# Optimization experiments

Measured on AMD Instinct MI355X. Metric: run time of the kernel, lower is better.

Reference implementation:

```python
import jax, jax.numpy as jnp
import numpy as np

# Dims: B=32 batch, C=64 feat channels, Np=192 priors, No=72 row offsets,
# Ns=36 pooled sample points (maxpool kernel 2), Hd=64 fc hidden.
B, C, Np, No, Hd = 32, 64, 192, 72, 64
NS_POOL = 2  # n_offsets // sample_points
REG_DIM = No + 4  # reg_layers output


def bilinear_sample(feat, gx, gy):
    """torch F.grid_sample(align_corners=True) equivalent for in-range coords.
    feat: [B,C,H,W]; gx,gy: [B,Np,S] normalized to [-1,1]. -> [B,C,Np,S]."""
    Bb, Cc, H, W = feat.shape
    ix = (gx + 1.0) * 0.5 * (W - 1)
    iy = (gy + 1.0) * 0.5 * (H - 1)
    ix0f = jnp.floor(ix); iy0f = jnp.floor(iy)
    wx = ix - ix0f; wy = iy - iy0f
    ix0 = jnp.clip(ix0f.astype(jnp.int32), 0, W - 1)
    iy0 = jnp.clip(iy0f.astype(jnp.int32), 0, H - 1)
    ix1 = jnp.clip(ix0 + 1, 0, W - 1)
    iy1 = jnp.clip(iy0 + 1, 0, H - 1)
    ff = feat.reshape(Bb, Cc, H * W)
    S = gx.shape[1] * gx.shape[2]
    def gather(iy_, ix_):
        idx = (iy_ * W + ix_).reshape(Bb, 1, S)
        g = jnp.take_along_axis(ff, jnp.broadcast_to(idx, (Bb, Cc, S)), axis=2)
        return g.reshape(Bb, Cc, gx.shape[1], gx.shape[2])
    v00 = gather(iy0, ix0); v01 = gather(iy0, ix1)
    v10 = gather(iy1, ix0); v11 = gather(iy1, ix1)
    wx = wx[:, None]; wy = wy[:, None]  # broadcast over C
    return (v00 * (1 - wx) * (1 - wy) + v01 * wx * (1 - wy)
            + v10 * (1 - wx) * wy + v11 * wx * wy)


def _mlp2(h, Ws, bs):
    # two stacked Linear+ReLU layers (num_fc=2)
    for i in range(2):
        h = jax.nn.relu(h @ Ws[i] + bs[i])
    return h


def setup_inputs() -> dict:
    key = jax.random.key(0)
    ks = jax.random.split(key, 24)
    w = lambda k, sh: jax.random.normal(k, sh, dtype=jnp.float32) * 0.05
    return {
        "x0": jax.random.normal(ks[0], (B, C, 40, 100), dtype=jnp.float32),
        "x1": jax.random.normal(ks[1], (B, C, 20, 50), dtype=jnp.float32),
        "x2": jax.random.normal(ks[2], (B, C, 10, 25), dtype=jnp.float32),
        "prior_xs0": jax.random.uniform(ks[3], (Np, No), dtype=jnp.float32),
        "l_weight": w(ks[4], (No,)),              # self.l embedding, sigmoid gate
        "lsgi_w": w(ks[5], (3, C, C)),            # per-stage lsgi projection
        "fc_w": w(ks[6], (C, Hd)), "fc_b": w(ks[7], (Hd,)),
        "cls_w": w(ks[8], (2, Hd, Hd)), "cls_b": w(ks[9], (2, Hd)),
        "cls_ow": w(ks[10], (Hd, 2)), "cls_ob": w(ks[11], (2,)),
        "reg_w": w(ks[12], (2, Hd, Hd)), "reg_b": w(ks[13], (2, Hd)),
        "reg_ow": w(ks[14], (Hd, REG_DIM)), "reg_ob": w(ks[15], (REG_DIM,)),
        "loc_w": w(ks[16], (2, Hd, Hd)), "loc_b": w(ks[17], (2, Hd)),
        "loc_ow": w(ks[18], (Hd, 1)), "loc_ob": w(ks[19], (1,)),
    }


def reference(x0, x1, x2, prior_xs0, l_weight, lsgi_w, fc_w, fc_b,
              cls_w, cls_b, cls_ow, cls_ob, reg_w, reg_b, reg_ow, reg_ob,
              loc_w, loc_b, loc_ow, loc_ob):
    pyramid = [x2, x1, x0]  # reversed: coarsest level first (stage 0)
    prior_feat_ys = jnp.linspace(1.0, 0.0, No, dtype=jnp.float32)
    gy = jnp.broadcast_to((prior_feat_ys * 2.0 - 1.0)[None, None, :], (B, Np, No))
    prior_xs = jnp.broadcast_to(prior_xs0[None], (B, Np, No))
    gate = jax.nn.sigmoid(l_weight)[:, None]  # [No,1]
    stage_feats = []
    outs = []
    for s in range(3):
        gx = prior_xs * 2.0 - 1.0
        pooled = bilinear_sample(pyramid[s], gx, gy)          # [B,C,Np,No]
        pooled = jnp.transpose(pooled, (0, 2, 3, 1)) * gate   # [B,Np,No,C]
        pooled = jax.nn.relu(jnp.einsum('bnoc,cd->bnod', pooled, lsgi_w[s]))
        # MaxPool2d kernel (2,1) over the offset axis -> Ns=36 sample points
        comp = pooled.reshape(B, Np, No // NS_POOL, NS_POOL, C).max(axis=3)
        stage_feats.append(comp)
        # cross-stage fusion (global head): mean over stages and sample points
        fused = jnp.stack(stage_feats, 0).mean(axis=0).mean(axis=2)  # [B,Np,C]
        fc = jax.nn.relu(fused @ fc_w + fc_b)                        # [B,Np,Hd]
        cls = _mlp2(fc, cls_w, cls_b) @ cls_ow + cls_ob              # [B,Np,2]
        reg = _mlp2(fc, reg_w, reg_b) @ reg_ow + reg_ob              # [B,Np,No+4]
        loc = _mlp2(fc, loc_w, loc_b) @ loc_ow + loc_ob              # [B,Np,1]
        outs.append(jnp.concatenate([cls, reg, loc], axis=-1))      # [B,Np,79]
        # refine anchors for next stage from predicted xs
        prior_xs = jax.nn.sigmoid(reg[..., 4:])
    return jnp.stack(outs, axis=0)  # [3,B,Np,79]
```

## Files before the change

kernel.cpp:

```cpp
#include <hip/hip_runtime.h>
#include <hip/hip_bf16.h>

#define Bq   32
#define Cq   64
#define NPq  192
#define NOq  72
#define PTS  (NPq * NOq)
#define REGD 76
#define OUTD 79

typedef __attribute__((ext_vector_type(8))) short short8;
typedef __attribute__((ext_vector_type(4))) float float4v;

__device__ inline unsigned short f2bf(float x) {
    __hip_bfloat16 h = __float2bfloat16(x);
    return *reinterpret_cast<unsigned short*>(&h);
}

__global__ __launch_bounds__(256) void build_tables_kernel(
    const float* __restrict__ f0,
    const float* __restrict__ f1,
    const float* __restrict__ f2,
    const float* __restrict__ lw,
    unsigned short* __restrict__ t0,
    unsigned short* __restrict__ t1,
    unsigned short* __restrict__ t2)
{
    __shared__ float sRow[64 * 101];

    const int tid = threadIdx.x;
    const int o   = blockIdx.x / 96;
    const int sb  = blockIdx.x - o * 96;
    const int s   = sb >> 5;
    const int b   = sb & 31;

    const float* feat; unsigned short* tab; int H, W;
    if (s == 0)      { feat = f0; tab = t0; H = 10; W = 25; }
    else if (s == 1) { feat = f1; tab = t1; H = 20; W = 50; }
    else             { feat = f2; tab = t2; H = 40; W = 100; }
    const int Wp = W + 1;

    const float ys = 1.0f - (float)o * (1.0f / 71.0f);
    const float iy = ys * (float)(H - 1);
    const float fy = floorf(iy);
    const float wy = iy - fy;
    int iy0 = (int)fy; iy0 = iy0 < 0 ? 0 : (iy0 > H - 1 ? H - 1 : iy0);
    const int iy1 = (iy0 + 1 > H - 1) ? H - 1 : iy0 + 1;
    const float gate = 1.0f / (1.0f + __expf(-lw[o]));

    const float* fb = feat + (size_t)b * 64 * H * W;
    const int iy0W = iy0 * W, iy1W = iy1 * W;

    const int tot = 64 * W;
    for (int idx = tid; idx < tot; idx += 256) {
        const int c = idx / W;
        const int x = idx - c * W;
        const float* f = fb + c * (H * W);
        sRow[c * Wp + x] = ((1.0f - wy) * f[iy0W + x] + wy * f[iy1W + x]) * gate;
    }
    __syncthreads();

    unsigned short* to = tab + (size_t)(b * NOq + o) * Wp * 64;
    const int tot2 = Wp * 64;
    for (int idx = tid; idx < tot2; idx += 256) {
        const int x = idx >> 6;
        const int c = idx & 63;
        const int xx = (x < W) ? x : (W - 1);
        to[idx] = f2bf(sRow[c * Wp + xx]);
    }
}

template<int W>
__global__ __launch_bounds__(256) void fused_pool_head_kernel(
    const unsigned short* __restrict__ tab,
    const float* __restrict__ xsrc, const int xstride,
    const float* __restrict__ lsgi,
    float* __restrict__ sumFeat,
    const int stage,
    const float* __restrict__ fc_w,  const float* __restrict__ fc_b,
    const float* __restrict__ cls_w, const float* __restrict__ cls_b,
    const float* __restrict__ cls_ow, const float* __restrict__ cls_ob,
    const float* __restrict__ reg_w, const float* __restrict__ reg_b,
    const float* __restrict__ reg_ow, const float* __restrict__ reg_ob,
    const float* __restrict__ loc_w, const float* __restrict__ loc_b,
    const float* __restrict__ loc_ow, const float* __restrict__ loc_ob,
    float* __restrict__ out, float* __restrict__ xs_next)
{
    constexpr int Wp = W + 1;
    __shared__ __align__(16) float sF  [8][68];
    __shared__ __align__(16) float bufC[8][64];
    __shared__ __align__(16) float bufA[8][64];
    __shared__ __align__(16) float bufB[8][64];

    const int tid  = threadIdx.x;
    const int w    = tid >> 6;
    const int lane = tid & 63;
    const int ng   = blockIdx.x >> 5;
    const int b    = blockIdx.x & 31;
    const int npair = ng * 4 + w;

    short8 wf[4][2];
    {
        const int kb = ((lane >> 4) & 3) * 8;
        const int dl = lane & 15;
        #pragma unroll
        for (int ks = 0; ks < 2; ++ks)
            #pragma unroll
            for (int dt = 0; dt < 4; ++dt) {
                union { unsigned short u[8]; short8 v; } pk;
                #pragma unroll
                for (int j = 0; j < 8; ++j)
                    pk.u[j] = f2bf(lsgi[(ks * 32 + kb + j) * 64 + dt * 16 + dl]);
                wf[dt][ks] = pk.v;
            }
    }

    const unsigned short* tb = tab + (size_t)b * NOq * Wp * 64;
    const float* xp = xsrc + (size_t)xstride * b;
    const int m  = lane & 15;
    const int kg = lane >> 4;
    const int nt0 = npair * 9;

    float sums0[4] = {0.f, 0.f, 0.f, 0.f};
    float sums1[4] = {0.f, 0.f, 0.f, 0.f};

    #pragma unroll
    for (int ntl = 0; ntl < 9; ++ntl) {
        const int pt = (nt0 + ntl) * 16 + m;
        const int o  = pt % NOq;
        float ixf = xp[pt] * (float)(W - 1);
        ixf = fminf(fmaxf(ixf, 0.0f), (float)(W - 1));
        const float fx = floorf(ixf);
        const float wx = ixf - fx;
        const int ix0 = (int)fx;

        const unsigned short* col = tb + ((size_t)o * Wp + ix0) * 64 + kg * 8;
        const short8 a00 = *(const short8*)(col);
        const short8 a01 = *(const short8*)(col + 64);
        const short8 a10 = *(const short8*)(col + 32);
        const short8 a11 = *(const short8*)(col + 96);

        float wxr[4];
        #pragma unroll
        for (int j = 0; j < 4; ++j) wxr[j] = __shfl(wx, kg * 4 + j);

        const bool hi = (ntl * 16 + (kg * 4)) >= NOq;
        #pragma unroll
        for (int dt = 0; dt < 4; ++dt) {
            float4v c0 = {0.f, 0.f, 0.f, 0.f};
            float4v c1 = {0.f, 0.f, 0.f, 0.f};
            c0 = __builtin_amdgcn_mfma_f32_16x16x32_bf16(a00, wf[dt][0], c0, 0, 0, 0);
            c0 = __builtin_amdgcn_mfma_f32_16x16x32_bf16(a10, wf[dt][1], c0, 0, 0, 0);
            c1 = __builtin_amdgcn_mfma_f32_16x16x32_bf16(a01, wf[dt][0], c1, 0, 0, 0);
            c1 = __builtin_amdgcn_mfma_f32_16x16x32_bf16(a11, wf[dt][1], c1, 0, 0, 0);
            const float v0 = c0[0] + wxr[0] * (c1[0] - c0[0]);
            const float v1 = c0[1] + wxr[1] * (c1[1] - c0[1]);
            const float v2 = c0[2] + wxr[2] * (c1[2] - c0[2]);
            const float v3 = c0[3] + wxr[3] * (c1[3] - c0[3]);
            const float pm0 = fmaxf(fmaxf(v0, v1), 0.f);
            const float pm1 = fmaxf(fmaxf(v2, v3), 0.f);
            const float add = pm0 + pm1;
            if (hi) sums1[dt] += add; else sums0[dt] += add;
        }
    }

    #pragma unroll
    for (int dt = 0; dt < 4; ++dt) {
        float v0 = sums0[dt], v1 = sums1[dt];
        v0 += __shfl_xor(v0, 16); v0 += __shfl_xor(v0, 32);
        v1 += __shfl_xor(v1, 16); v1 += __shfl_xor(v1, 32);
        sums0[dt] = v0; sums1[dt] = v1;
    }

    const float invS = 1.0f / (float)(stage + 1);
    if (lane < 16) {
        const size_t row0 = (size_t)(b * NPq + npair * 2) * 64;
        #pragma unroll
        for (int dt = 0; dt < 4; ++dt) {
            const int d = dt * 16 + lane;
            float t0 = sums0[dt] * (1.0f / 36.0f);
            float t1 = sums1[dt] * (1.0f / 36.0f);
            float* p0 = sumFeat + row0 + d;
            float* p1 = sumFeat + row0 + 64 + d;
            if (stage > 0) { t0 += *p0; t1 += *p1; }
            *p0 = t0; *p1 = t1;
            sF[2 * w][d]     = t0 * invS;
            sF[2 * w + 1][d] = t1 * invS;
        }
    }
    __syncthreads();

    const int pA  = w;
    const int pB  = w + 4;
    const int p0g = b * NPq + ng * 8;

    auto layer = [&](const float* iA, const float* iB, float* oA, float* oB,
                     const float* __restrict__ gw, const float* __restrict__ gb) {
        const float bias = gb[lane];
        float accA = bias, accB = bias;
        #pragma unroll 4
        for (int k = 0; k < 64; k += 4) {
            const float4 a4 = *(const float4*)(iA + k);
            const float4 b4 = *(const float4*)(iB + k);
            const float w0 = gw[(k + 0) * 64 + lane];
            const float w1 = gw[(k + 1) * 64 + lane];
            const float w2 = gw[(k + 2) * 64 + lane];
            const float w3 = gw[(k + 3) * 64 + lane];
            accA += a4.x * w0 + a4.y * w1 + a4.z * w2 + a4.w * w3;
            accB += b4.x * w0 + b4.y * w1 + b4.z * w2 + b4.w * w3;
        }
        oA[lane] = fmaxf(accA, 0.f);
        oB[lane] = fmaxf(accB, 0.f);
        __builtin_amdgcn_wave_barrier();
    };

    layer(sF[pA], sF[pB], bufC[pA], bufC[pB], fc_w, fc_b);

    layer(bufC[pA], bufC[pB], bufA[pA], bufA[pB], cls_w,        cls_b);
    layer(bufA[pA], bufA[pB], bufB[pA], bufB[pB], cls_w + 4096, cls_b + 64);
    {
        const float bA = bufB[pA][lane], bB = bufB[pB][lane];
        const float2 ow = *(const float2*)&cls_ow[lane * 2];
        float v0 = bA * ow.x, v1 = bA * ow.y;
        float v2 = bB * ow.x, v3 = bB * ow.y;
        #pragma unroll
        for (int m2 = 1; m2 < 64; m2 <<= 1) {
            v0 += __shfl_xor(v0, m2);
            v1 += __shfl_xor(v1, m2);
            v2 += __shfl_xor(v2, m2);
            v3 += __shfl_xor(v3, m2);
        }
        if (lane == 0) {
            out[(size_t)(p0g + pA) * OUTD + 0] = v0 + cls_ob[0];
            out[(size_t)(p0g + pA) * OUTD + 1] = v1 + cls_ob[1];
            out[(size_t)(p0g + pB) * OUTD + 0] = v2 + cls_ob[0];
            out[(size_t)(p0g + pB) * OUTD + 1] = v3 + cls_ob[1];
        }
    }

    layer(bufC[pA], bufC[pB], bufA[pA], bufA[pB], reg_w,        reg_b);
    layer(bufA[pA], bufA[pB], bufB[pA], bufB[pB], reg_w + 4096, reg_b + 64);
    {
        const int j1 = lane;
        const int j2 = (lane < 12) ? 64 + lane : 75;
        float zA1 = reg_ob[j1], zB1 = zA1;
        float zA2 = reg_ob[j2], zB2 = zA2;
        #pragma unroll 4
        for (int k = 0; k < 64; k += 4) {
            const float4 a4 = *(const float4*)&bufB[pA][k];
            const float4 b4 = *(const float4*)&bufB[pB][k];
            const float u0 = reg_ow[(k + 0) * REGD + j1];
            const float u1 = reg_ow[(k + 1) * REGD + j1];
            const float u2 = reg_ow[(k + 2) * REGD + j1];
            const float u3 = reg_ow[(k + 3) * REGD + j1];
            const float t0 = reg_ow[(k + 0) * REGD + j2];
            const float t1 = reg_ow[(k + 1) * REGD + j2];
            const float t2 = reg_ow[(k + 2) * REGD + j2];
            const float t3 = reg_ow[(k + 3) * REGD + j2];
            zA1 += a4.x * u0 + a4.y * u1 + a4.z * u2 + a4.w * u3;
            zB1 += b4.x * u0 + b4.y * u1 + b4.z * u2 + b4.w * u3;
            zA2 += a4.x * t0 + a4.y * t1 + a4.z * t2 + a4.w * t3;
            zB2 += b4.x * t0 + b4.y * t1 + b4.z * t2 + b4.w * t3;
        }
        float* orA = out + (size_t)(p0g + pA) * OUTD;
        float* orB = out + (size_t)(p0g + pB) * OUTD;
        float* xsA = xs_next + (size_t)(p0g + pA) * NOq;
        float* xsB = xs_next + (size_t)(p0g + pB) * NOq;
        orA[2 + j1] = zA1;
        orB[2 + j1] = zB1;
        if (lane >= 4) {
            xsA[j1 - 4] = 1.0f / (1.0f + __expf(-zA1));
            xsB[j1 - 4] = 1.0f / (1.0f + __expf(-zB1));
        }
        if (lane < 12) {
            orA[2 + j2] = zA2;
            orB[2 + j2] = zB2;
            xsA[j2 - 4] = 1.0f / (1.0f + __expf(-zA2));
            xsB[j2 - 4] = 1.0f / (1.0f + __expf(-zB2));
        }
    }

    layer(bufC[pA], bufC[pB], bufA[pA], bufA[pB], loc_w,        loc_b);
    layer(bufA[pA], bufA[pB], bufB[pA], bufB[pB], loc_w + 4096, loc_b + 64);
    {
        float v0 = bufB[pA][lane] * loc_ow[lane];
        float v1 = bufB[pB][lane] * loc_ow[lane];
        #pragma unroll
        for (int m2 = 1; m2 < 64; m2 <<= 1) {
            v0 += __shfl_xor(v0, m2);
            v1 += __shfl_xor(v1, m2);
        }
        if (lane == 0) {
            out[(size_t)(p0g + pA) * OUTD + 78] = v0 + loc_ob[0];
            out[(size_t)(p0g + pB) * OUTD + 78] = v1 + loc_ob[0];
        }
    }
}

extern "C" void kernel_launch(void* const* d_in, const int* in_sizes, int n_in,
                              void* d_out, int out_size, void* d_ws, size_t ws_size,
                              hipStream_t stream)
{
    const float* x0        = (const float*)d_in[0];
    const float* x1        = (const float*)d_in[1];
    const float* x2        = (const float*)d_in[2];
    const float* prior_xs0 = (const float*)d_in[3];
    const float* l_weight  = (const float*)d_in[4];
    const float* lsgi_w    = (const float*)d_in[5];
    const float* fc_w      = (const float*)d_in[6];
    const float* fc_b      = (const float*)d_in[7];
    const float* cls_w     = (const float*)d_in[8];
    const float* cls_b     = (const float*)d_in[9];
    const float* cls_ow    = (const float*)d_in[10];
    const float* cls_ob    = (const float*)d_in[11];
    const float* reg_w     = (const float*)d_in[12];
    const float* reg_b     = (const float*)d_in[13];
    const float* reg_ow    = (const float*)d_in[14];
    const float* reg_ob    = (const float*)d_in[15];
    const float* loc_w     = (const float*)d_in[16];
    const float* loc_b     = (const float*)d_in[17];
    const float* loc_ow    = (const float*)d_in[18];
    const float* loc_ob    = (const float*)d_in[19];

    float* out     = (float*)d_out;
    float* sumFeat = (float*)d_ws;
    float* xs      = sumFeat + (size_t)Bq * NPq * Cq;
    unsigned short* tab0 = (unsigned short*)(xs + (size_t)Bq * PTS);
    unsigned short* tab1 = tab0 + (size_t)Bq * NOq * 26  * 64;
    unsigned short* tab2 = tab1 + (size_t)Bq * NOq * 51  * 64;

    hipLaunchKernelGGL(build_tables_kernel, dim3(3 * Bq * NOq), dim3(256), 0, stream,
                       x2, x1, x0, l_weight, tab0, tab1, tab2);

    for (int s = 0; s < 3; ++s) {
        const float* xsrc = (s == 0) ? prior_xs0 : xs;
        const int xstr    = (s == 0) ? 0 : PTS;
        const unsigned short* tb = (s == 0) ? tab0 : (s == 1) ? tab1 : tab2;
        float* outS = out + (size_t)s * Bq * NPq * OUTD;
        if (s == 0)
            hipLaunchKernelGGL((fused_pool_head_kernel<25>), dim3(Bq * 24), dim3(256), 0, stream,
                               tb, xsrc, xstr, lsgi_w + s * 4096, sumFeat, s,
                               fc_w, fc_b, cls_w, cls_b, cls_ow, cls_ob,
                               reg_w, reg_b, reg_ow, reg_ob,
                               loc_w, loc_b, loc_ow, loc_ob, outS, xs);
        else if (s == 1)
            hipLaunchKernelGGL((fused_pool_head_kernel<50>), dim3(Bq * 24), dim3(256), 0, stream,
                               tb, xsrc, xstr, lsgi_w + s * 4096, sumFeat, s,
                               fc_w, fc_b, cls_w, cls_b, cls_ow, cls_ob,
                               reg_w, reg_b, reg_ow, reg_ob,
                               loc_w, loc_b, loc_ow, loc_ob, outS, xs);
        else
            hipLaunchKernelGGL((fused_pool_head_kernel<100>), dim3(Bq * 24), dim3(256), 0, stream,
                               tb, xsrc, xstr, lsgi_w + s * 4096, sumFeat, s,
                               fc_w, fc_b, cls_w, cls_b, cls_ow, cls_ob,
                               reg_w, reg_b, reg_ow, reg_ob,
                               loc_w, loc_b, loc_ow, loc_ob, outS, xs);
    }
}
```

Measured before the change: 244.4 us.

## Double waves per block, splitting output channels and head rows across waves

Measured after the change: 303.5 us. 1.24x slower.

```diff
diff --git a/kernel.cpp b/kernel.cpp
--- a/kernel.cpp
+++ b/kernel.cpp
@@ -71,7 +71,7 @@
 }
 
 template<int W>
-__global__ __launch_bounds__(256) void fused_pool_head_kernel(
+__global__ __launch_bounds__(512) void fused_pool_head_kernel(
     const unsigned short* __restrict__ tab,
     const float* __restrict__ xsrc, const int xstride,
     const float* __restrict__ lsgi,
@@ -97,21 +97,23 @@
     const int lane = tid & 63;
     const int ng   = blockIdx.x >> 5;
     const int b    = blockIdx.x & 31;
-    const int npair = ng * 4 + w;
-
-    short8 wf[4][2];
+    const int q    = w & 3;
+    const int d0   = (w >> 2) * 2;
+    const int npair = ng * 4 + q;
+
+    short8 wf[2][2];
     {
         const int kb = ((lane >> 4) & 3) * 8;
         const int dl = lane & 15;
         #pragma unroll
         for (int ks = 0; ks < 2; ++ks)
             #pragma unroll
-            for (int dt = 0; dt < 4; ++dt) {
+            for (int t = 0; t < 2; ++t) {
                 union { unsigned short u[8]; short8 v; } pk;
                 #pragma unroll
                 for (int j = 0; j < 8; ++j)
-                    pk.u[j] = f2bf(lsgi[(ks * 32 + kb + j) * 64 + dt * 16 + dl]);
-                wf[dt][ks] = pk.v;
+                    pk.u[j] = f2bf(lsgi[(ks * 32 + kb + j) * 64 + (d0 + t) * 16 + dl]);
+                wf[t][ks] = pk.v;
             }
     }
 
@@ -121,8 +123,8 @@
     const int kg = lane >> 4;
     const int nt0 = npair * 9;
 
-    float sums0[4] = {0.f, 0.f, 0.f, 0.f};
-    float sums1[4] = {0.f, 0.f, 0.f, 0.f};
+    float sums0[2] = {0.f, 0.f};
+    float sums1[2] = {0.f, 0.f};
 
     #pragma unroll
     for (int ntl = 0; ntl < 9; ++ntl) {
@@ -146,13 +148,13 @@
 
         const bool hi = (ntl * 16 + (kg * 4)) >= NOq;
         #pragma unroll
-        for (int dt = 0; dt < 4; ++dt) {
+        for (int t = 0; t < 2; ++t) {
             float4v c0 = {0.f, 0.f, 0.f, 0.f};
             float4v c1 = {0.f, 0.f, 0.f, 0.f};
-            c0 = __builtin_amdgcn_mfma_f32_16x16x32_bf16(a00, wf[dt][0], c0, 0, 0, 0);
-            c0 = __builtin_amdgcn_mfma_f32_16x16x32_bf16(a10, wf[dt][1], c0, 0, 0, 0);
-            c1 = __builtin_amdgcn_mfma_f32_16x16x32_bf16(a01, wf[dt][0], c1, 0, 0, 0);
-            c1 = __builtin_amdgcn_mfma_f32_16x16x32_bf16(a11, wf[dt][1], c1, 0, 0, 0);
+            c0 = __builtin_amdgcn_mfma_f32_16x16x32_bf16(a00, wf[t][0], c0, 0, 0, 0);
+            c0 = __builtin_amdgcn_mfma_f32_16x16x32_bf16(a10, wf[t][1], c0, 0, 0, 0);
+            c1 = __builtin_amdgcn_mfma_f32_16x16x32_bf16(a01, wf[t][0], c1, 0, 0, 0);
+            c1 = __builtin_amdgcn_mfma_f32_16x16x32_bf16(a11, wf[t][1], c1, 0, 0, 0);
             const float v0 = c0[0] + wxr[0] * (c1[0] - c0[0]);
             const float v1 = c0[1] + wxr[1] * (c1[1] - c0[1]);
             const float v2 = c0[2] + wxr[2] * (c1[2] - c0[2]);
@@ -160,140 +162,104 @@
             const float pm0 = fmaxf(fmaxf(v0, v1), 0.f);
             const float pm1 = fmaxf(fmaxf(v2, v3), 0.f);
             const float add = pm0 + pm1;
-            if (hi) sums1[dt] += add; else sums0[dt] += add;
+            if (hi) sums1[t] += add; else sums0[t] += add;
         }
     }
 
     #pragma unroll
-    for (int dt = 0; dt < 4; ++dt) {
-        float v0 = sums0[dt], v1 = sums1[dt];
+    for (int t = 0; t < 2; ++t) {
+        float v0 = sums0[t], v1 = sums1[t];
         v0 += __shfl_xor(v0, 16); v0 += __shfl_xor(v0, 32);
         v1 += __shfl_xor(v1, 16); v1 += __shfl_xor(v1, 32);
-        sums0[dt] = v0; sums1[dt] = v1;
+        sums0[t] = v0; sums1[t] = v1;
     }
 
     const float invS = 1.0f / (float)(stage + 1);
     if (lane < 16) {
         const size_t row0 = (size_t)(b * NPq + npair * 2) * 64;
         #pragma unroll
-        for (int dt = 0; dt < 4; ++dt) {
-            const int d = dt * 16 + lane;
-            float t0 = sums0[dt] * (1.0f / 36.0f);
-            float t1 = sums1[dt] * (1.0f / 36.0f);
+        for (int t = 0; t < 2; ++t) {
+            const int d = (d0 + t) * 16 + lane;
+            float t0 = sums0[t] * (1.0f / 36.0f);
+            float t1 = sums1[t] * (1.0f / 36.0f);
             float* p0 = sumFeat + row0 + d;
             float* p1 = sumFeat + row0 + 64 + d;
             if (stage > 0) { t0 += *p0; t1 += *p1; }
             *p0 = t0; *p1 = t1;
-            sF[2 * w][d]     = t0 * invS;
-            sF[2 * w + 1][d] = t1 * invS;
+            sF[2 * q][d]     = t0 * invS;
+            sF[2 * q + 1][d] = t1 * invS;
         }
     }
     __syncthreads();
 
-    const int pA  = w;
-    const int pB  = w + 4;
     const int p0g = b * NPq + ng * 8;
 
-    auto layer = [&](const float* iA, const float* iB, float* oA, float* oB,
+    auto layer = [&](const float* iA, float* oA,
                      const float* __restrict__ gw, const float* __restrict__ gb) {
-        const float bias = gb[lane];
-        float accA = bias, accB = bias;
+        float acc = gb[lane];
         #pragma unroll 4
         for (int k = 0; k < 64; k += 4) {
             const float4 a4 = *(const float4*)(iA + k);
-            const float4 b4 = *(const float4*)(iB + k);
-            const float w0 = gw[(k + 0) * 64 + lane];
-            const float w1 = gw[(k + 1) * 64 + lane];
-            const float w2 = gw[(k + 2) * 64 + lane];
-            const float w3 = gw[(k + 3) * 64 + lane];
-            accA += a4.x * w0 + a4.y * w1 + a4.z * w2 + a4.w * w3;
-            accB += b4.x * w0 + b4.y * w1 + b4.z * w2 + b4.w * w3;
-        }
-        oA[lane] = fmaxf(accA, 0.f);
-        oB[lane] = fmaxf(accB, 0.f);
+            acc += a4.x * gw[(k + 0) * 64 + lane]
+                 + a4.y * gw[(k + 1) * 64 + lane]
+                 + a4.z * gw[(k + 2) * 64 + lane]
+                 + a4.w * gw[(k + 3) * 64 + lane];
+        }
+        oA[lane] = fmaxf(acc, 0.f);
         __builtin_amdgcn_wave_barrier();
     };
 
-    layer(sF[pA], sF[pB], bufC[pA], bufC[pB], fc_w, fc_b);
-
-    layer(bufC[pA], bufC[pB], bufA[pA], bufA[pB], cls_w,        cls_b);
-    layer(bufA[pA], bufA[pB], bufB[pA], bufB[pB], cls_w + 4096, cls_b + 64);
+    layer(sF[w], bufC[w], fc_w, fc_b);
+
+    layer(bufC[w], bufA[w], cls_w,        cls_b);
+    layer(bufA[w], bufB[w], cls_w + 4096, cls_b + 64);
     {
-        const float bA = bufB[pA][lane], bB = bufB[pB][lane];
+        const float bA = bufB[w][lane];
         const float2 ow = *(const float2*)&cls_ow[lane * 2];
         float v0 = bA * ow.x, v1 = bA * ow.y;
-        float v2 = bB * ow.x, v3 = bB * ow.y;
         #pragma unroll
         for (int m2 = 1; m2 < 64; m2 <<= 1) {
             v0 += __shfl_xor(v0, m2);
             v1 += __shfl_xor(v1, m2);
-            v2 += __shfl_xor(v2, m2);
-            v3 += __shfl_xor(v3, m2);
         }
         if (lane == 0) {
-            out[(size_t)(p0g + pA) * OUTD + 0] = v0 + cls_ob[0];
-            out[(size_t)(p0g + pA) * OUTD + 1] = v1 + cls_ob[1];
-            out[(size_t)(p0g + pB) * OUTD + 0] = v2 + cls_ob[0];
-            out[(size_t)(p0g + pB) * OUTD + 1] = v3 + cls_ob[1];
-        }
-    }
-
-    layer(bufC[pA], bufC[pB], bufA[pA], bufA[pB], reg_w,        reg_b);
-    layer(bufA[pA], bufA[pB], bufB[pA], bufB[pB], reg_w + 4096, reg_b + 64);
+            out[(size_t)(p0g + w) * OUTD + 0] = v0 + cls_ob[0];
+            out[(size_t)(p0g + w) * OUTD + 1] = v1 + cls_ob[1];
+        }
+    }
+
+    layer(bufC[w], bufA[w], reg_w,        reg_b);
+    layer(bufA[w], bufB[w], reg_w + 4096, reg_b + 64);
     {
         const int j1 = lane;
         const int j2 = (lane < 12) ? 64 + lane : 75;
-        float zA1 = reg_ob[j1], zB1 = zA1;
-        float zA2 = reg_ob[j2], zB2 = zA2;
+        float zA1 = reg_ob[j1];
+        float zA2 = reg_ob[j2];
         #pragma unroll 4
         for (int k = 0; k < 64; k += 4) {
-            const float4 a4 = *(const float4*)&bufB[pA][k];
-            const float4 b4 = *(const float4*)&bufB[pB][k];
-            const float u0 = reg_ow[(k + 0) * REGD + j1];
-            const float u1 = reg_ow[(k + 1) * REGD + j1];
-            const float u2 = reg_ow[(k + 2) * REGD + j1];
-            const float u3 = reg_ow[(k + 3) * REGD + j1];
-            const float t0 = reg_ow[(k + 0) * REGD + j2];
-            const float t1 = reg_ow[(k + 1) * REGD + j2];
-            const float t2 = reg_ow[(k + 2) * REGD + j2];
-            const float t3 = reg_ow[(k + 3) * REGD + j2];
-            zA1 += a4.x * u0 + a4.y * u1 + a4.z * u2 + a4.w * u3;
-            zB1 += b4.x * u0 + b4.y * u1 + b4.z * u2 + b4.w * u3;
-            zA2 += a4.x * t0 + a4.y * t1 + a4.z * t2 + a4.w * t3;
-            zB2 += b4.x * t0 + b4.y * t1 + b4.z * t2 + b4.w * t3;
-        }
-        float* orA = out + (size_t)(p0g + pA) * OUTD;
-        float* orB = out + (size_t)(p0g + pB) * OUTD;
-        float* xsA = xs_next + (size_t)(p0g + pA) * NOq;
-        float* xsB = xs_next + (size_t)(p0g + pB) * NOq;
+            const float4 a4 = *(const float4*)&bufB[w][k];
+            zA1 += a4.x * reg_ow[(k + 0) * REGD + j1] + a4.y * reg_ow[(k + 1) * REGD + j1]
+                 + a4.z * reg_ow[(k + 2) * REGD + j1] + a4.w * reg_ow[(k + 3) * REGD + j1];
+            zA2 += a4.x * reg_ow[(k + 0) * REGD + j2] + a4.y * reg_ow[(k + 1) * REGD + j2]
+                 + a4.z * reg_ow[(k + 2) * REGD + j2] + a4.w * reg_ow[(k + 3) * REGD + j2];
+        }
+        float* orA = out + (size_t)(p0g + w) * OUTD;
+        float* xsA = xs_next + (size_t)(p0g + w) * NOq;
         orA[2 + j1] = zA1;
-        orB[2 + j1] = zB1;
-        if (lane >= 4) {
-            xsA[j1 - 4] = 1.0f / (1.0f + __expf(-zA1));
-            xsB[j1 - 4] = 1.0f / (1.0f + __expf(-zB1));
-        }
+        if (lane >= 4) xsA[j1 - 4] = 1.0f / (1.0f + __expf(-zA1));
         if (lane < 12) {
             orA[2 + j2] = zA2;
-            orB[2 + j2] = zB2;
             xsA[j2 - 4] = 1.0f / (1.0f + __expf(-zA2));
-            xsB[j2 - 4] = 1.0f / (1.0f + __expf(-zB2));
-        }
-    }
-
-    layer(bufC[pA], bufC[pB], bufA[pA], bufA[pB], loc_w,        loc_b);
-    layer(bufA[pA], bufA[pB], bufB[pA], bufB[pB], loc_w + 4096, loc_b + 64);
+        }
+    }
+
+    layer(bufC[w], bufA[w], loc_w,        loc_b);
+    layer(bufA[w], bufB[w], loc_w + 4096, loc_b + 64);
     {
-        float v0 = bufB[pA][lane] * loc_ow[lane];
-        float v1 = bufB[pB][lane] * loc_ow[lane];
-        #pragma unroll
-        for (int m2 = 1; m2 < 64; m2 <<= 1) {
-            v0 += __shfl_xor(v0, m2);
-            v1 += __shfl_xor(v1, m2);
-        }
-        if (lane == 0) {
-            out[(size_t)(p0g + pA) * OUTD + 78] = v0 + loc_ob[0];
-            out[(size_t)(p0g + pB) * OUTD + 78] = v1 + loc_ob[0];
-        }
+        float v0 = bufB[w][lane] * loc_ow[lane];
+        #pragma unroll
+        for (int m2 = 1; m2 < 64; m2 <<= 1) v0 += __shfl_xor(v0, m2);
+        if (lane == 0) out[(size_t)(p0g + w) * OUTD + 78] = v0 + loc_ob[0];
     }
 }
 
@@ -338,19 +304,19 @@
         const unsigned short* tb = (s == 0) ? tab0 : (s == 1) ? tab1 : tab2;
         float* outS = out + (size_t)s * Bq * NPq * OUTD;
         if (s == 0)
-            hipLaunchKernelGGL((fused_pool_head_kernel<25>), dim3(Bq * 24), dim3(256), 0, stream,
+            hipLaunchKernelGGL((fused_pool_head_kernel<25>), dim3(Bq * 24), dim3(512), 0, stream,
                                tb, xsrc, xstr, lsgi_w + s * 4096, sumFeat, s,
                                fc_w, fc_b, cls_w, cls_b, cls_ow, cls_ob,
                                reg_w, reg_b, reg_ow, reg_ob,
                                loc_w, loc_b, loc_ow, loc_ob, outS, xs);
         else if (s == 1)
-            hipLaunchKernelGGL((fused_pool_head_kernel<50>), dim3(Bq * 24), dim3(256), 0, stream,
+            hipLaunchKernelGGL((fused_pool_head_kernel<50>), dim3(Bq * 24), dim3(512), 0, stream,
                                tb, xsrc, xstr, lsgi_w + s * 4096, sumFeat, s,
                                fc_w, fc_b, cls_w, cls_b, cls_ow, cls_ob,
                                reg_w, reg_b, reg_ow, reg_ob,
                                loc_w, loc_b, loc_ow, loc_ob, outS, xs);
         else
-            hipLaunchKernelGGL((fused_pool_head_kernel<100>), dim3(Bq * 24), dim3(256), 0, stream,
+            hipLaunchKernelGGL((fused_pool_head_kernel<100>), dim3(Bq * 24), dim3(512), 0, stream,
                                tb, xsrc, xstr, lsgi_w + s * 4096, sumFeat, s,
                                fc_w, fc_b, cls_w, cls_b, cls_ow, cls_ob,
                                reg_w, reg_b, reg_ow, reg_ob,
```

## Split pooling of each prior pair across two waves and double grid size

Applied to the files above, without the earlier changes.

Result: slower. 278.4 us (+13.9%).

```diff
diff --git a/kernel.cpp b/kernel.cpp
--- a/kernel.cpp
+++ b/kernel.cpp
@@ -87,17 +87,20 @@
     float* __restrict__ out, float* __restrict__ xs_next)
 {
     constexpr int Wp = W + 1;
-    __shared__ __align__(16) float sF  [8][68];
-    __shared__ __align__(16) float bufC[8][64];
-    __shared__ __align__(16) float bufA[8][64];
-    __shared__ __align__(16) float bufB[8][64];
+    __shared__ __align__(16) float sF  [4][68];
+    __shared__ __align__(16) float bufC[4][64];
+    __shared__ __align__(16) float bufA[4][64];
+    __shared__ __align__(16) float bufB[4][64];
+    __shared__ __align__(16) float sPart[2][2][4][2][16];
 
     const int tid  = threadIdx.x;
     const int w    = tid >> 6;
     const int lane = tid & 63;
     const int ng   = blockIdx.x >> 5;
     const int b    = blockIdx.x & 31;
-    const int npair = ng * 4 + w;
+    const int npi  = w >> 1;
+    const int half = w & 1;
+    const int npair = ng * 2 + npi;
 
     short8 wf[4][2];
     {
@@ -124,8 +127,7 @@
     float sums0[4] = {0.f, 0.f, 0.f, 0.f};
     float sums1[4] = {0.f, 0.f, 0.f, 0.f};
 
-    #pragma unroll
-    for (int ntl = 0; ntl < 9; ++ntl) {
+    auto poolIter = [&](const int ntl) {
         const int pt = (nt0 + ntl) * 16 + m;
         const int o  = pt % NOq;
         float ixf = xp[pt] * (float)(W - 1);
@@ -162,6 +164,14 @@
             const float add = pm0 + pm1;
             if (hi) sums1[dt] += add; else sums0[dt] += add;
         }
+    };
+
+    if (half == 0) {
+        #pragma unroll
+        for (int ntl = 0; ntl < 5; ++ntl) poolIter(ntl);
+    } else {
+        #pragma unroll
+        for (int ntl = 5; ntl < 9; ++ntl) poolIter(ntl);
     }
 
     #pragma unroll
@@ -172,27 +182,38 @@
         sums0[dt] = v0; sums1[dt] = v1;
     }
 
+    if (lane < 16) {
+        #pragma unroll
+        for (int dt = 0; dt < 4; ++dt) {
+            sPart[npi][half][dt][0][lane] = sums0[dt];
+            sPart[npi][half][dt][1][lane] = sums1[dt];
+        }
+    }
+    __syncthreads();
+
     const float invS = 1.0f / (float)(stage + 1);
-    if (lane < 16) {
+    if (half == 0 && lane < 16) {
         const size_t row0 = (size_t)(b * NPq + npair * 2) * 64;
         #pragma unroll
         for (int dt = 0; dt < 4; ++dt) {
             const int d = dt * 16 + lane;
-            float t0 = sums0[dt] * (1.0f / 36.0f);
-            float t1 = sums1[dt] * (1.0f / 36.0f);
+            float t0 = (sPart[npi][0][dt][0][lane] + sPart[npi][1][dt][0][lane]) * (1.0f / 36.0f);
+            float t1 = (sPart[npi][0][dt][1][lane] + sPart[npi][1][dt][1][lane]) * (1.0f / 36.0f);
             float* p0 = sumFeat + row0 + d;
             float* p1 = sumFeat + row0 + 64 + d;
             if (stage > 0) { t0 += *p0; t1 += *p1; }
             *p0 = t0; *p1 = t1;
-            sF[2 * w][d]     = t0 * invS;
-            sF[2 * w + 1][d] = t1 * invS;
+            sF[2 * npi][d]     = t0 * invS;
+            sF[2 * npi + 1][d] = t1 * invS;
         }
     }
     __syncthreads();
 
+    if (w >= 2) return;
+
     const int pA  = w;
-    const int pB  = w + 4;
-    const int p0g = b * NPq + ng * 8;
+    const int pB  = w + 2;
+    const int p0g = b * NPq + ng * 4;
 
     auto layer = [&](const float* iA, const float* iB, float* oA, float* oB,
                      const float* __restrict__ gw, const float* __restrict__ gb) {
@@ -338,19 +359,19 @@
         const unsigned short* tb = (s == 0) ? tab0 : (s == 1) ? tab1 : tab2;
         float* outS = out + (size_t)s * Bq * NPq * OUTD;
         if (s == 0)
-            hipLaunchKernelGGL((fused_pool_head_kernel<25>), dim3(Bq * 24), dim3(256), 0, stream,
+            hipLaunchKernelGGL((fused_pool_head_kernel<25>), dim3(Bq * 48), dim3(256), 0, stream,
                                tb, xsrc, xstr, lsgi_w + s * 4096, sumFeat, s,
                                fc_w, fc_b, cls_w, cls_b, cls_ow, cls_ob,
                                reg_w, reg_b, reg_ow, reg_ob,
                                loc_w, loc_b, loc_ow, loc_ob, outS, xs);
         else if (s == 1)
-            hipLaunchKernelGGL((fused_pool_head_kernel<50>), dim3(Bq * 24), dim3(256), 0, stream,
+            hipLaunchKernelGGL((fused_pool_head_kernel<50>), dim3(Bq * 48), dim3(256), 0, stream,
                                tb, xsrc, xstr, lsgi_w + s * 4096, sumFeat, s,
                                fc_w, fc_b, cls_w, cls_b, cls_ow, cls_ob,
                                reg_w, reg_b, reg_ow, reg_ob,
                                loc_w, loc_b, loc_ow, loc_ob, outS, xs);
         else
-            hipLaunchKernelGGL((fused_pool_head_kernel<100>), dim3(Bq * 24), dim3(256), 0, stream,
+            hipLaunchKernelGGL((fused_pool_head_kernel<100>), dim3(Bq * 48), dim3(256), 0, stream,
                                tb, xsrc, xstr, lsgi_w + s * 4096, sumFeat, s,
                                fc_w, fc_b, cls_w, cls_b, cls_ow, cls_ob,
                                reg_w, reg_b, reg_ow, reg_ob,
```
